# Optimization experiments

Hardware: AMD Instinct MI355X
Metric: run time of the kernel (lower is better)

## Reference

```python
import jax, jax.numpy as jnp
import numpy as np

EPS = 1e-8

def unit_normalize(x):
    # x / max(||x||_2, eps) along last dim (matches F.normalize semantics)
    n = jnp.sqrt(jnp.sum(x * x, axis=-1, keepdims=True))
    return x / jnp.maximum(n, EPS)

def setup_inputs() -> dict:
    key = jax.random.key(0)
    k1, k2, k3, k4 = jax.random.split(key, 4)
    BS, N, B, r, D = 8, 4096, 8, 64, 256
    q = jax.random.normal(k1, (BS, N, B, D), dtype=jnp.float32)
    pm_K = unit_normalize(jax.random.normal(k2, (BS, B, r, D), dtype=jnp.float32))
    pm_V = jax.random.normal(k3, (BS, B, r, D), dtype=jnp.float32)
    pm_a = jax.random.uniform(k4, (BS, B, r), dtype=jnp.float32)
    return {"q": q, "pm_K": pm_K, "pm_V": pm_V, "pm_a": pm_a}

def reference(q, pm_K, pm_V, pm_a):
    # Holographic read: q [BS,N,B,D], pm_K/pm_V [BS,B,r,D], pm_a [BS,B,r]
    q_norm = unit_normalize(q)
    # scores = normalize(q) @ pm_K^T  -> [BS,N,B,r]
    scores = jnp.einsum('snbd,sbrd->snbr', q_norm, pm_K)
    # slot-strength scaling
    weighted = scores * pm_a[:, None, :, :]
    # modulation = weighted @ pm_V -> [BS,N,B,D]
    modulation = jnp.einsum('snbr,sbrd->snbd', weighted, pm_V)
    return q * modulation
```

## Files before the change

kernel.cpp:

```cpp
#include <hip/hip_runtime.h>

#define BS 8
#define NN 4096
#define NB 8
#define NR 64
#define ND 256
#define TN 128
#define QPAD 264
#define SPAD 72

typedef __attribute__((ext_vector_type(8))) short bf16x8;
typedef __attribute__((ext_vector_type(4))) float f32x4;

__device__ __forceinline__ unsigned short f2bf(float f) {
    unsigned int u = __builtin_bit_cast(unsigned int, f);
    u += 0x7fffu + ((u >> 16) & 1u);
    return (unsigned short)(u >> 16);
}
__device__ __forceinline__ float bf2f(unsigned short h) {
    unsigned int u = ((unsigned int)h) << 16;
    return __builtin_bit_cast(float, u);
}

__global__ __launch_bounds__(512, 2)
void holo_read_kernel(const float* __restrict__ q,
                      const float* __restrict__ pmK,
                      const float* __restrict__ pmV,
                      const float* __restrict__ pma,
                      float* __restrict__ out)
{
    __shared__ __attribute__((aligned(16))) unsigned short qbf[TN][QPAD];
    __shared__ __attribute__((aligned(16))) unsigned short Kb[NR][QPAD];
    __shared__ __attribute__((aligned(16))) unsigned short Vt[ND][SPAD];
    __shared__ __attribute__((aligned(16))) unsigned short Ssm[TN][SPAD];
    __shared__ float a_sh[NR];

    const int tid  = threadIdx.x;
    const int lane = tid & 63;
    const int w    = tid >> 6;
    const int ln15 = lane & 15;
    const int quad = lane >> 4;

    const int sbi   = blockIdx.x & 63;
    const int chunk = blockIdx.x >> 6;
    const int s     = sbi >> 3;
    const int b     = sbi & 7;

    const int myrow = w * 16 + ln15;
    const size_t row_stride = (size_t)NB * ND;
    const float* qbase = q   + ((size_t)(s * NN + chunk * 1024 + myrow) * NB + b) * ND + quad * 8;
    float*       obase = out + ((size_t)(s * NN + chunk * 1024 + myrow) * NB + b) * ND;

    float4 pf[16];
    {
        const float* p = qbase;
        #pragma unroll
        for (int kk = 0; kk < 8; ++kk) {
            pf[2 * kk]     = *(const float4*)(p + kk * 32);
            pf[2 * kk + 1] = *(const float4*)(p + kk * 32 + 4);
        }
    }

    if (tid < NR) a_sh[tid] = pma[sbi * NR + tid];
    const size_t kvbase = (size_t)sbi * NR * ND;
    for (int rr = w; rr < NR; rr += 8) {
        const float4 kv = *(const float4*)&pmK[kvbase + (size_t)rr * ND + lane * 4];
        ushort4 uk;
        uk.x = f2bf(kv.x); uk.y = f2bf(kv.y); uk.z = f2bf(kv.z); uk.w = f2bf(kv.w);
        *(ushort4*)&Kb[rr][lane * 4] = uk;
        const float4 vv = *(const float4*)&pmV[kvbase + (size_t)rr * ND + lane * 4];
        Vt[lane * 4 + 0][rr] = f2bf(vv.x);
        Vt[lane * 4 + 1][rr] = f2bf(vv.y);
        Vt[lane * 4 + 2][rr] = f2bf(vv.z);
        Vt[lane * 4 + 3][rr] = f2bf(vv.w);
    }
    __syncthreads();

    float ar[4];
    #pragma unroll
    for (int rt = 0; rt < 4; ++rt) ar[rt] = a_sh[rt * 16 + ln15];

    for (int it = 0; it < 8; ++it) {
        float ss = 0.f;
        bf16x8 qfrag[8];
        #pragma unroll
        for (int kk = 0; kk < 8; ++kk) {
            const float4 v0 = pf[2 * kk], v1 = pf[2 * kk + 1];
            ss += v0.x * v0.x + v0.y * v0.y + v0.z * v0.z + v0.w * v0.w
                + v1.x * v1.x + v1.y * v1.y + v1.z * v1.z + v1.w * v1.w;
            bf16x8 f;
            f[0] = (short)f2bf(v0.x); f[1] = (short)f2bf(v0.y);
            f[2] = (short)f2bf(v0.z); f[3] = (short)f2bf(v0.w);
            f[4] = (short)f2bf(v1.x); f[5] = (short)f2bf(v1.y);
            f[6] = (short)f2bf(v1.z); f[7] = (short)f2bf(v1.w);
            qfrag[kk] = f;
            *(bf16x8*)&qbf[myrow][kk * 32 + quad * 8] = f;
        }

        if (it < 7) {
            const float* p = qbase + (size_t)(it + 1) * 128 * row_stride;
            #pragma unroll
            for (int kk = 0; kk < 8; ++kk) {
                pf[2 * kk]     = *(const float4*)(p + kk * 32);
                pf[2 * kk + 1] = *(const float4*)(p + kk * 32 + 4);
            }
        }

        ss += __shfl_xor(ss, 16, 64);
        ss += __shfl_xor(ss, 32, 64);
        const float inv = 1.0f / fmaxf(sqrtf(ss), 1e-8f);

        f32x4 accS[4];
        #pragma unroll
        for (int rt = 0; rt < 4; ++rt) accS[rt] = (f32x4){0.f, 0.f, 0.f, 0.f};
        #pragma unroll
        for (int kk = 0; kk < 8; ++kk) {
            #pragma unroll
            for (int rt = 0; rt < 4; ++rt) {
                const bf16x8 bfr = *(const bf16x8*)&Kb[rt * 16 + ln15][kk * 32 + quad * 8];
                accS[rt] = __builtin_amdgcn_mfma_f32_16x16x32_bf16(qfrag[kk], bfr, accS[rt], 0, 0, 0);
            }
        }
        #pragma unroll
        for (int rt = 0; rt < 4; ++rt) {
            #pragma unroll
            for (int reg = 0; reg < 4; ++reg) {
                Ssm[w * 16 + quad * 4 + reg][rt * 16 + ln15] = f2bf(accS[rt][reg] * ar[rt]);
            }
        }

        f32x4 accO[16];
        #pragma unroll
        for (int dt = 0; dt < 16; ++dt) accO[dt] = (f32x4){0.f, 0.f, 0.f, 0.f};
        #pragma unroll
        for (int kt = 0; kt < 2; ++kt) {
            const bf16x8 aw = *(const bf16x8*)&Ssm[myrow][kt * 32 + quad * 8];
            #pragma unroll
            for (int dt = 0; dt < 16; ++dt) {
                const bf16x8 bv = *(const bf16x8*)&Vt[dt * 16 + ln15][kt * 32 + quad * 8];
                accO[dt] = __builtin_amdgcn_mfma_f32_16x16x32_bf16(bv, aw, accO[dt], 0, 0, 0);
            }
        }

        float* op = obase + (size_t)it * 128 * row_stride;
        #pragma unroll
        for (int dt = 0; dt < 16; ++dt) {
            const ushort4 qb = *(const ushort4*)&qbf[myrow][dt * 16 + quad * 4];
            float4 o;
            o.x = bf2f(qb.x) * (inv * accO[dt][0]);
            o.y = bf2f(qb.y) * (inv * accO[dt][1]);
            o.z = bf2f(qb.z) * (inv * accO[dt][2]);
            o.w = bf2f(qb.w) * (inv * accO[dt][3]);
            *(float4*)(op + dt * 16 + quad * 4) = o;
        }
    }
}

extern "C" void kernel_launch(void* const* d_in, const int* in_sizes, int n_in,
                              void* d_out, int out_size, void* d_ws, size_t ws_size,
                              hipStream_t stream) {
    const float* q   = (const float*)d_in[0];
    const float* pmK = (const float*)d_in[1];
    const float* pmV = (const float*)d_in[2];
    const float* pma = (const float*)d_in[3];
    float* out = (float*)d_out;
    (void)in_sizes; (void)n_in; (void)out_size; (void)d_ws; (void)ws_size;
    hipLaunchKernelGGL(holo_read_kernel, dim3(256), dim3(512), 0, stream,
                       q, pmK, pmV, pma, out);
}
```

Baseline: 551.6 us.

## Interleave score MFMAs with bf16 conversion and split output GEMM into halves

Issues the score MFMAs inside the q conversion loop, so the qfrag array no longer has to be held across the prefetch. The second GEMM and the epilogue are split into two halves of 8 d-tiles each, which halves the live accO registers. sched_barrier calls are added to stop the compiler from reordering across phases. The aim is to cut register pressure so the two blocks per CU allowed by launch bounds fit without spills. The barriers may also limit latency hiding between the prefetch loads and the compute.

```diff
diff --git a/kernel.cpp b/kernel.cpp
--- a/kernel.cpp
+++ b/kernel.cpp
@@ -82,7 +82,10 @@
 
     for (int it = 0; it < 8; ++it) {
         float ss = 0.f;
-        bf16x8 qfrag[8];
+        f32x4 accS[4];
+        #pragma unroll
+        for (int rt = 0; rt < 4; ++rt) accS[rt] = (f32x4){0.f, 0.f, 0.f, 0.f};
+
         #pragma unroll
         for (int kk = 0; kk < 8; ++kk) {
             const float4 v0 = pf[2 * kk], v1 = pf[2 * kk + 1];
@@ -93,9 +96,17 @@
             f[2] = (short)f2bf(v0.z); f[3] = (short)f2bf(v0.w);
             f[4] = (short)f2bf(v1.x); f[5] = (short)f2bf(v1.y);
             f[6] = (short)f2bf(v1.z); f[7] = (short)f2bf(v1.w);
-            qfrag[kk] = f;
             *(bf16x8*)&qbf[myrow][kk * 32 + quad * 8] = f;
+            #pragma unroll
+            for (int rt = 0; rt < 4; ++rt) {
+                const bf16x8 bfr = *(const bf16x8*)&Kb[rt * 16 + ln15][kk * 32 + quad * 8];
+                accS[rt] = __builtin_amdgcn_mfma_f32_16x16x32_bf16(f, bfr, accS[rt], 0, 0, 0);
+            }
         }
+
+        ss += __shfl_xor(ss, 16, 64);
+        ss += __shfl_xor(ss, 32, 64);
+        const float inv = 1.0f / fmaxf(sqrtf(ss), 1e-8f);
 
         if (it < 7) {
             const float* p = qbase + (size_t)(it + 1) * 128 * row_stride;
@@ -105,22 +116,8 @@
                 pf[2 * kk + 1] = *(const float4*)(p + kk * 32 + 4);
             }
         }
+        __builtin_amdgcn_sched_barrier(0);
 
-        ss += __shfl_xor(ss, 16, 64);
-        ss += __shfl_xor(ss, 32, 64);
-        const float inv = 1.0f / fmaxf(sqrtf(ss), 1e-8f);
-
-        f32x4 accS[4];
-        #pragma unroll
-        for (int rt = 0; rt < 4; ++rt) accS[rt] = (f32x4){0.f, 0.f, 0.f, 0.f};
-        #pragma unroll
-        for (int kk = 0; kk < 8; ++kk) {
-            #pragma unroll
-            for (int rt = 0; rt < 4; ++rt) {
-                const bf16x8 bfr = *(const bf16x8*)&Kb[rt * 16 + ln15][kk * 32 + quad * 8];
-                accS[rt] = __builtin_amdgcn_mfma_f32_16x16x32_bf16(qfrag[kk], bfr, accS[rt], 0, 0, 0);
-            }
-        }
         #pragma unroll
         for (int rt = 0; rt < 4; ++rt) {
             #pragma unroll
@@ -129,29 +126,58 @@
             }
         }
 
-        f32x4 accO[16];
-        #pragma unroll
-        for (int dt = 0; dt < 16; ++dt) accO[dt] = (f32x4){0.f, 0.f, 0.f, 0.f};
-        #pragma unroll
-        for (int kt = 0; kt < 2; ++kt) {
-            const bf16x8 aw = *(const bf16x8*)&Ssm[myrow][kt * 32 + quad * 8];
+        const bf16x8 aw0 = *(const bf16x8*)&Ssm[myrow][quad * 8];
+        const bf16x8 aw1 = *(const bf16x8*)&Ssm[myrow][32 + quad * 8];
+
+        float* op = obase + (size_t)it * 128 * row_stride;
+
+        {
+            f32x4 accO[8];
             #pragma unroll
-            for (int dt = 0; dt < 16; ++dt) {
-                const bf16x8 bv = *(const bf16x8*)&Vt[dt * 16 + ln15][kt * 32 + quad * 8];
-                accO[dt] = __builtin_amdgcn_mfma_f32_16x16x32_bf16(bv, aw, accO[dt], 0, 0, 0);
+            for (int i = 0; i < 8; ++i) accO[i] = (f32x4){0.f, 0.f, 0.f, 0.f};
+            #pragma unroll
+            for (int dt = 0; dt < 8; ++dt) {
+                const bf16x8 bv0 = *(const bf16x8*)&Vt[dt * 16 + ln15][quad * 8];
+                const bf16x8 bv1 = *(const bf16x8*)&Vt[dt * 16 + ln15][32 + quad * 8];
+                accO[dt] = __builtin_amdgcn_mfma_f32_16x16x32_bf16(bv0, aw0, accO[dt], 0, 0, 0);
+                accO[dt] = __builtin_amdgcn_mfma_f32_16x16x32_bf16(bv1, aw1, accO[dt], 0, 0, 0);
+            }
+            #pragma unroll
+            for (int dt = 0; dt < 8; ++dt) {
+                const ushort4 qb = *(const ushort4*)&qbf[myrow][dt * 16 + quad * 4];
+                float4 o;
+                o.x = bf2f(qb.x) * (inv * accO[dt][0]);
+                o.y = bf2f(qb.y) * (inv * accO[dt][1]);
+                o.z = bf2f(qb.z) * (inv * accO[dt][2]);
+                o.w = bf2f(qb.w) * (inv * accO[dt][3]);
+                *(float4*)(op + dt * 16 + quad * 4) = o;
             }
         }
+        __builtin_amdgcn_sched_barrier(0);
 
-        float* op = obase + (size_t)it * 128 * row_stride;
-        #pragma unroll
-        for (int dt = 0; dt < 16; ++dt) {
-            const ushort4 qb = *(const ushort4*)&qbf[myrow][dt * 16 + quad * 4];
-            float4 o;
-            o.x = bf2f(qb.x) * (inv * accO[dt][0]);
-            o.y = bf2f(qb.y) * (inv * accO[dt][1]);
-            o.z = bf2f(qb.z) * (inv * accO[dt][2]);
-            o.w = bf2f(qb.w) * (inv * accO[dt][3]);
-            *(float4*)(op + dt * 16 + quad * 4) = o;
+        {
+            f32x4 accO[8];
+            #pragma unroll
+            for (int i = 0; i < 8; ++i) accO[i] = (f32x4){0.f, 0.f, 0.f, 0.f};
+            #pragma unroll
+            for (int dt8 = 0; dt8 < 8; ++dt8) {
+                const int dt = dt8 + 8;
+                const bf16x8 bv0 = *(const bf16x8*)&Vt[dt * 16 + ln15][quad * 8];
+                const bf16x8 bv1 = *(const bf16x8*)&Vt[dt * 16 + ln15][32 + quad * 8];
+                accO[dt8] = __builtin_amdgcn_mfma_f32_16x16x32_bf16(bv0, aw0, accO[dt8], 0, 0, 0);
+                accO[dt8] = __builtin_amdgcn_mfma_f32_16x16x32_bf16(bv1, aw1, accO[dt8], 0, 0, 0);
+            }
+            #pragma unroll
+            for (int dt8 = 0; dt8 < 8; ++dt8) {
+                const int dt = dt8 + 8;
+                const ushort4 qb = *(const ushort4*)&qbf[myrow][dt * 16 + quad * 4];
+                float4 o;
+                o.x = bf2f(qb.x) * (inv * accO[dt8][0]);
+                o.y = bf2f(qb.y) * (inv * accO[dt8][1]);
+                o.z = bf2f(qb.z) * (inv * accO[dt8][2]);
+                o.w = bf2f(qb.w) * (inv * accO[dt8][3]);
+                *(float4*)(op + dt * 16 + quad * 4) = o;
+            }
         }
     }
 }
```

New measurement: 456.9 us. 1.21x faster.
